# Kernel optimization log

Hardware: AMD Instinct MI355X
Metric: run time of the kernel (lower is better)

Reference implementation:

```python
import jax, jax.numpy as jnp
import numpy as np

N, D, H, C, K = 16384, 128, 128, 10, 32  # cells, in-dim, hidden, classes, kNN neighbors


def setup_inputs() -> dict:
    key = jax.random.key(0)
    k0, k1, k2 = jax.random.split(key, 3)
    return {
        "X": jax.random.normal(k0, (N, D), dtype=jnp.float32),
        "W1": jax.random.normal(k1, (2 * D, H), dtype=jnp.float32) * 0.05,
        "b1": jnp.zeros((H,), dtype=jnp.float32),
        "W2": jax.random.normal(k2, (2 * H, C), dtype=jnp.float32) * 0.05,
        "b2": jnp.zeros((C,), dtype=jnp.float32),
    }


def _knn_idx(X, k):
    # knn_graph(X, k, loop=True): k nearest neighbors incl. self per node
    sq = jnp.sum(X * X, axis=1)
    d2 = sq[:, None] - 2.0 * (X @ X.T) + sq[None, :]  # [N, N] squared dists
    _, idx = jax.lax.top_k(-d2, k)  # [N, k] neighbor indices (self has d2=0)
    return idx


def _edge_conv(X, idx, W, b, relu):
    # PyG EdgeConv: out_i = max_j mlp(concat(x_i, x_j - x_i))
    xi = X[:, None, :]                 # [N, 1, d]
    xj = X[idx]                        # [N, k, d] gather
    msg = jnp.concatenate([jnp.broadcast_to(xi, xj.shape), xj - xi], axis=-1)
    h = msg @ W + b                    # [N, k, out]
    if relu:
        h = jax.nn.relu(h)
    return jnp.max(h, axis=1)          # max aggregation over neighbors


def reference(X, W1, b1, W2, b2):
    # dropout p=0.0 -> identity
    idx = _knn_idx(X, K)               # graph built once, reused (edge_index cached)
    h = _edge_conv(X, idx, W1, b1, relu=True)
    out = _edge_conv(h, idx, W2, b2, relu=False)
    return out
```

## Files before the change

### kernel.cpp

```cpp
#include <hip/hip_runtime.h>
#include <math.h>

#define Nn 16384
#define Dd 128
#define Kk 32
#define JSPLIT 8
#define JCH (Nn / JSPLIT)
#define NG (JCH / 16)
#define CAP 32
#define MAXSLOT 2
#define BAND 0.4f
#define ZQ 2.4176f

typedef unsigned short u16;
typedef short short8 __attribute__((ext_vector_type(8)));
typedef float f32x4 __attribute__((ext_vector_type(4)));

__device__ __forceinline__ u16 f2bf(float x) {
    unsigned u = __float_as_uint(x);
    unsigned r = u + 0x7FFFu + ((u >> 16) & 1u);
    return (u16)(r >> 16);
}

__global__ __launch_bounds__(256) void prep_kernel(const float* __restrict__ X,
                                                   u16* __restrict__ Xhi,
                                                   float* __restrict__ sqn,
                                                   float* __restrict__ thrA,
                                                   int* __restrict__ flagCnt) {
    const int i = blockIdx.x * 4 + (threadIdx.x >> 6);
    const int lane = threadIdx.x & 63;
    const float2 v = *(const float2*)(X + (size_t)i * Dd + lane * 2);
    const unsigned pack = ((unsigned)f2bf(v.y) << 16) | (unsigned)f2bf(v.x);
    *(unsigned*)(Xhi + (size_t)i * Dd + lane * 2) = pack;
    float s = fmaf(v.x, v.x, v.y * v.y);
#pragma unroll
    for (int o = 32; o > 0; o >>= 1) s += __shfl_down(s, o);
    if (lane == 0) {
        sqn[i] = s;
        thrA[i] = 128.0f - ZQ * sqrtf(256.0f + 4.0f * s);
    }
    if (blockIdx.x == 0 && threadIdx.x == 0) *flagCnt = 0;
}

__global__ __launch_bounds__(256, 2) void knn_filter(const u16* __restrict__ Xhi,
                                                     const float* __restrict__ sqn,
                                                     const float* __restrict__ thrA,
                                                     u16* __restrict__ cand,
                                                     int* __restrict__ candCnt) {
    __shared__ u16 listF[256 * CAP + 256];
    __shared__ int cntS[256];

    const int tid = threadIdx.x;
    const int wave = tid >> 6, lane = tid & 63;
    const int quad = lane >> 4, n16 = lane & 15;
    const int itile = blockIdx.x >> 3, chunk = blockIdx.x & 7;
    const int ibase = itile * 256;
    const int wbase = ibase + wave * 64;
    const int jch0 = chunk * JCH;
    const unsigned below = (1u << n16) - 1u;
    const int scrapOff = 256 * CAP + tid;

    short8 aF[4][4];
#pragma unroll
    for (int is = 0; is < 4; is++) {
        const u16* arow = Xhi + (size_t)(wbase + is * 16 + n16) * Dd + quad * 8;
#pragma unroll
        for (int ks = 0; ks < 4; ks++) aF[is][ks] = *(const short8*)(arow + ks * 32);
    }
    float nhT[16];
    int cntReg[16];
#pragma unroll
    for (int is = 0; is < 4; is++)
#pragma unroll
        for (int r = 0; r < 4; r++) {
            nhT[is * 4 + r] = -0.5f * thrA[wbase + is * 16 + quad * 4 + r];
            cntReg[is * 4 + r] = 0;
        }

    const u16* bbase = Xhi + (size_t)(jch0 + n16) * Dd + quad * 8;
    short8 bb[2][4];
    float sj[2];
#pragma unroll
    for (int ks = 0; ks < 4; ks++) bb[0][ks] = *(const short8*)(bbase + ks * 32);
    sj[0] = sqn[jch0 + n16];
#pragma unroll
    for (int ks = 0; ks < 4; ks++) bb[1][ks] = *(const short8*)(bbase + 16 * Dd + ks * 32);
    sj[1] = sqn[jch0 + 16 + n16];

#define MSTEP(p, gg)                                                           \
    {                                                                          \
        const float bias = -0.5f * sj[p];                                      \
        acc##p[0] = (f32x4){bias, bias, bias, bias};                           \
        acc##p[1] = acc##p[0]; acc##p[2] = acc##p[0]; acc##p[3] = acc##p[0];   \
        _Pragma("unroll")                                                      \
        for (int ks = 0; ks < 4; ks++) {                                       \
            acc##p[0] = __builtin_amdgcn_mfma_f32_16x16x32_bf16(aF[0][ks], bb[p][ks], acc##p[0], 0, 0, 0); \
            acc##p[1] = __builtin_amdgcn_mfma_f32_16x16x32_bf16(aF[1][ks], bb[p][ks], acc##p[1], 0, 0, 0); \
            acc##p[2] = __builtin_amdgcn_mfma_f32_16x16x32_bf16(aF[2][ks], bb[p][ks], acc##p[2], 0, 0, 0); \
            acc##p[3] = __builtin_amdgcn_mfma_f32_16x16x32_bf16(aF[3][ks], bb[p][ks], acc##p[3], 0, 0, 0); \
        }                                                                      \
        {      \
            const u16* nb = bbase + (size_t)((gg) + 2) * 16 * Dd;              \
            bb[p][0] = *(const short8*)(nb);                                   \
            bb[p][1] = *(const short8*)(nb + 32);                              \
            bb[p][2] = *(const short8*)(nb + 64);                              \
            bb[p][3] = *(const short8*)(nb + 96);                              \
            sj[p] = sqn[jch0 + ((gg) + 2) * 16 + n16];                         \
        }                                                                      \
    }

#define TSTEP(p, gg)                                                           \
    {                                                                          \
        const int jj = jch0 + (gg) * 16 + n16;                                 \
        _Pragma("unroll")                                                      \
        for (int is = 0; is < 4; is++) {                                       \
            _Pragma("unroll")                                                  \
            for (int r = 0; r < 4; r++) {                                      \
                const int ir = is * 4 + r;                                     \
                const bool h = acc##p[is][r] > nhT[ir];                        \
                const unsigned long long mr = __ballot(h);                     \
                const unsigned qm = (unsigned)(mr >> (quad * 16)) & 0xFFFFu;   \
                const int pos = cntReg[ir] + __popc(qm & below);               \
                const bool wr = h && (pos < CAP);                              \
                const int rowbase = (wave * 64 + is * 16 + quad * 4 + r) * CAP; \
                const int off = wr ? rowbase + pos : scrapOff;                 \
                listF[off] = (u16)jj;        \
                cntReg[ir] += __popc(qm);                                      \
            }                                                                  \
        }                                                                      \
    }

    f32x4 acc0[4], acc1[4];
    MSTEP(0, 0)
    for (int g = 0; g < NG - 2; g += 2) {
        MSTEP(1, g + 1)
        TSTEP(0, g)
        MSTEP(0, g + 2)
        TSTEP(1, g + 1)
    }
    MSTEP(1, NG - 1)
    TSTEP(0, NG - 2)
    TSTEP(1, NG - 1)
#undef MSTEP
#undef TSTEP

    if (n16 == 0) {
#pragma unroll
        for (int is = 0; is < 4; is++)
#pragma unroll
            for (int r = 0; r < 4; r++)
                cntS[wave * 64 + is * 16 + quad * 4 + r] = cntReg[is * 4 + r];
    }
    for (int rl = 0; rl < 64; rl++) {
        const int row = wave * 64 + rl;
        const int n = cntS[row];
        const int gi = ibase + row;
        if (lane == 0) candCnt[(size_t)gi * JSPLIT + chunk] = n;
        if (lane < min(n, CAP))
            cand[((size_t)gi * JSPLIT + chunk) * CAP + lane] = listF[row * CAP + lane];
    }
}

__global__ __launch_bounds__(256) void knn_exact(const float* __restrict__ X,
                                                 const float* __restrict__ sqn,
                                                 const float* __restrict__ thrA,
                                                 const u16* __restrict__ cand,
                                                 const int* __restrict__ candCnt,
                                                 int* __restrict__ idx_out,
                                                 int* __restrict__ flagCnt,
                                                 int* __restrict__ flagRows) {
    const int wave = threadIdx.x >> 6, lane = threadIdx.x & 63;
    const int quad = lane >> 4, n16 = lane & 15;
    const int i = blockIdx.x * 4 + wave;

    float4 xi[8];
    {
        const float4* xb = (const float4*)(X + (size_t)i * Dd + quad * 32);
#pragma unroll
        for (int u = 0; u < 8; u++) xi[u] = xb[u];
    }
    int pre[JSPLIT];
    bool over = false;
    int M = 0;
#pragma unroll
    for (int k = 0; k < JSPLIT; k++) {
        int c = candCnt[(size_t)i * JSPLIT + k];
        over = over || (c > CAP);
        pre[k] = M;
        M += min(c, CAP);
    }
    over = over || (M > 64 * MAXSLOT);
    if (over) {
        if (lane == 0) { const int f = atomicAdd(flagCnt, 1); flagRows[f] = i; }
        return;
    }
    const float rvT = thrA[i];

    float rv[MAXSLOT];
    int jd[MAXSLOT];
#pragma unroll
    for (int s = 0; s < MAXSLOT; s++) { rv[s] = INFINITY; jd[s] = -1; }

#pragma unroll
    for (int s = 0; s < MAXSLOT; s++) {
#pragma unroll
        for (int t = 0; t < 4; t++) {
            const int c = s * 64 + t * 16 + n16;
            if (c < M) {
                int k = 0;
#pragma unroll
                for (int q = 1; q < JSPLIT; q++) if (c >= pre[q]) k = q;
                const int jj = cand[((size_t)i * JSPLIT + k) * CAP + (c - pre[k])];
                const float4* xb = (const float4*)(X + (size_t)jj * Dd + quad * 32);
                float s0 = 0.f, s1 = 0.f, s2 = 0.f, s3 = 0.f;
#pragma unroll
                for (int u = 0; u < 8; u++) {
                    const float4 b = xb[u];
                    s0 = fmaf(xi[u].x, b.x, s0); s1 = fmaf(xi[u].y, b.y, s1);
                    s2 = fmaf(xi[u].z, b.z, s2); s3 = fmaf(xi[u].w, b.w, s3);
                }
                float p = (s0 + s1) + (s2 + s3);
                p += __shfl_xor(p, 16);
                p += __shfl_xor(p, 32);
                if (quad == t) { rv[s] = fmaf(-2.f, p, sqn[jj]); jd[s] = jj; }
            }
        }
    }

    int good = 0;
#pragma unroll
    for (int s = 0; s < MAXSLOT; s++) good += __popcll(__ballot(rv[s] < rvT - BAND));
    if (good < Kk) {
        if (lane == 0) { const int f = atomicAdd(flagCnt, 1); flagRows[f] = i; }
        return;
    }
    int rk[MAXSLOT] = {};
    for (int s2 = 0; s2 < 64; s2++) {
        float ov[MAXSLOT];
#pragma unroll
        for (int s = 0; s < MAXSLOT; s++) ov[s] = __shfl(rv[s], s2);
#pragma unroll
        for (int s = 0; s < MAXSLOT; s++) {
            const int myid = lane + 64 * s;
#pragma unroll
            for (int t = 0; t < MAXSLOT; t++)
                rk[s] += (ov[t] < rv[s] || (ov[t] == rv[s] && s2 + 64 * t < myid)) ? 1 : 0;
        }
    }
#pragma unroll
    for (int s = 0; s < MAXSLOT; s++)
        if (jd[s] >= 0 && rk[s] < Kk) idx_out[(size_t)i * Kk + rk[s]] = jd[s];
}

__global__ __launch_bounds__(256) void knn_cleanup(const float* __restrict__ X,
                                                   const float* __restrict__ sqn,
                                                   const int* __restrict__ flagCnt,
                                                   const int* __restrict__ flagRows,
                                                   float* __restrict__ scratch,
                                                   int* __restrict__ idx_out) {
    __shared__ float xi[Dd];
    __shared__ int cntS;
    __shared__ float lv[256];
    __shared__ int lj[256];
    const int tid = threadIdx.x;
    const int lane = tid & 63;
    const int F = *flagCnt;
    float* rvS = scratch + (size_t)blockIdx.x * Nn;
    for (int f = blockIdx.x; f < F; f += gridDim.x) {
        const int i = flagRows[f];
        __syncthreads();
        if (tid < Dd) xi[tid] = X[(size_t)i * Dd + tid];
        __syncthreads();
        for (int j = tid; j < Nn; j += 256) {
            const float* xj = X + (size_t)j * Dd;
            float s0 = 0.f, s1 = 0.f, s2 = 0.f, s3 = 0.f;
#pragma unroll
            for (int d = 0; d < Dd; d += 4) {
                const float4 a = *(const float4*)&xi[d];
                const float4 b = *(const float4*)(xj + d);
                s0 = fmaf(a.x, b.x, s0); s1 = fmaf(a.y, b.y, s1);
                s2 = fmaf(a.z, b.z, s2); s3 = fmaf(a.w, b.w, s3);
            }
            rvS[j] = fmaf(-2.f, (s0 + s1) + (s2 + s3), sqn[j]);
        }
        __syncthreads();
        float lo = -1.0e9f, hi = 1.0e9f, T = 1.0e9f;
        for (int it = 0; it < 48; it++) {
            const float mid = 0.5f * (lo + hi);
            int local = 0;
            for (int j = tid; j < Nn; j += 256) local += (rvS[j] < mid) ? 1 : 0;
#pragma unroll
            for (int o = 32; o > 0; o >>= 1) local += __shfl_down(local, o);
            __syncthreads();
            if (tid == 0) cntS = 0;
            __syncthreads();
            if (lane == 0) atomicAdd(&cntS, local);
            __syncthreads();
            const int c = cntS;
            if (c < Kk) lo = mid;
            else if (c > 200) hi = mid;
            else { T = mid; break; }
        }
        if (T == 1.0e9f) T = hi;
        __syncthreads();
        if (tid == 0) cntS = 0;
        __syncthreads();
        for (int j = tid; j < Nn; j += 256) {
            if (rvS[j] < T) {
                const int p = atomicAdd(&cntS, 1);
                if (p < 256) { lv[p] = rvS[j]; lj[p] = j; }
            }
        }
        __syncthreads();
        const int n = min(cntS, 256);
        if (tid < 64) {
            float v[4]; int jjj[4]; int rk2[4] = {0, 0, 0, 0};
#pragma unroll
            for (int s = 0; s < 4; s++) {
                const int sl = lane + 64 * s;
                v[s] = (sl < n) ? lv[sl] : INFINITY;
                jjj[s] = (sl < n) ? lj[sl] : -1;
            }
            for (int s2 = 0; s2 < 64; s2++) {
                const float o0 = __shfl(v[0], s2), o1 = __shfl(v[1], s2);
                const float o2 = __shfl(v[2], s2), o3 = __shfl(v[3], s2);
#pragma unroll
                for (int s = 0; s < 4; s++) {
                    const int myid = lane + 64 * s;
                    rk2[s] += (o0 < v[s] || (o0 == v[s] && s2 < myid));
                    rk2[s] += (o1 < v[s] || (o1 == v[s] && s2 + 64 < myid));
                    rk2[s] += (o2 < v[s] || (o2 == v[s] && s2 + 128 < myid));
                    rk2[s] += (o3 < v[s] || (o3 == v[s] && s2 + 192 < myid));
                }
            }
#pragma unroll
            for (int s = 0; s < 4; s++)
                if (jjj[s] >= 0 && rk2[s] < Kk) idx_out[(size_t)i * Kk + rk2[s]] = jjj[s];
        }
        __syncthreads();
    }
}

__global__ __launch_bounds__(256) void pq_kernel(const float* __restrict__ X,
                                                 const float* __restrict__ W1,
                                                 const float* __restrict__ b1,
                                                 float* __restrict__ P,
                                                 float* __restrict__ Q) {
    __shared__ float xrow[16][Dd];
    const int i0 = blockIdx.x * 16;
    for (int t = threadIdx.x; t < 16 * Dd / 4; t += 256)
        ((float4*)&xrow[0][0])[t] = ((const float4*)(X + (size_t)i0 * Dd))[t];
    __syncthreads();
    const int cc = threadIdx.x & 127;
    const int mat = threadIdx.x >> 7;
    float acc[16];
#pragma unroll
    for (int r = 0; r < 16; r++) acc[r] = 0.f;
    for (int d = 0; d < Dd; d++) {
        float w;
        if (mat == 0) w = W1[d * 128 + cc] - W1[(128 + d) * 128 + cc];
        else          w = W1[(128 + d) * 128 + cc];
#pragma unroll
        for (int r = 0; r < 16; r++) acc[r] = fmaf(xrow[r][d], w, acc[r]);
    }
    if (mat == 0) {
        const float b = b1[cc];
#pragma unroll
        for (int r = 0; r < 16; r++) P[(size_t)(i0 + r) * 128 + cc] = acc[r] + b;
    } else {
#pragma unroll
        for (int r = 0; r < 16; r++) Q[(size_t)(i0 + r) * 128 + cc] = acc[r];
    }
}

__global__ __launch_bounds__(128) void h1_kernel(const float* __restrict__ P,
                                                 const float* __restrict__ Q,
                                                 const int* __restrict__ idx,
                                                 float* __restrict__ h1) {
    const int i = blockIdx.x;
    const int c = threadIdx.x;
    __shared__ int jb[Kk];
    if (threadIdx.x < Kk) jb[threadIdx.x] = idx[(size_t)i * Kk + threadIdx.x];
    __syncthreads();
    float m = -INFINITY;
#pragma unroll
    for (int k = 0; k < Kk; k++) m = fmaxf(m, Q[(size_t)jb[k] * 128 + c]);
    h1[(size_t)i * 128 + c] = fmaxf(P[(size_t)i * 128 + c] + m, 0.f);
}

__global__ __launch_bounds__(256) void pq2_kernel(const float* __restrict__ h1,
                                                  const float* __restrict__ W2,
                                                  const float* __restrict__ b2,
                                                  float* __restrict__ P2,
                                                  float* __restrict__ Q2) {
    __shared__ float w2s[2560];
    __shared__ float h1s[16][132];
    const int i0 = blockIdx.x * 16;
    for (int t = threadIdx.x; t < 640; t += 256)
        ((float4*)w2s)[t] = ((const float4*)W2)[t];
    {
        const int r = threadIdx.x >> 4, q = (threadIdx.x & 15) * 8;
        *(float4*)&h1s[r][q]     = *(const float4*)(h1 + (size_t)(i0 + r) * 128 + q);
        *(float4*)&h1s[r][q + 4] = *(const float4*)(h1 + (size_t)(i0 + r) * 128 + q + 4);
    }
    __syncthreads();
    const int il = threadIdx.x >> 4, c = threadIdx.x & 15;
    if (c >= 10) return;
    float pa = 0.f, pb = 0.f;
#pragma unroll 4
    for (int d = 0; d < Dd; d++) {
        const float h = h1s[il][d];
        const float wa = w2s[d * 10 + c];
        const float wb = w2s[(128 + d) * 10 + c];
        pa = fmaf(h, wa - wb, pa);
        pb = fmaf(h, wb, pb);
    }
    P2[(size_t)(i0 + il) * 10 + c] = pa + b2[c];
    Q2[(size_t)(i0 + il) * 10 + c] = pb;
}

__global__ __launch_bounds__(256) void out_kernel(const float* __restrict__ P2,
                                                  const float* __restrict__ Q2,
                                                  const int* __restrict__ idx,
                                                  float* __restrict__ out) {
    const int g = blockIdx.x * 256 + threadIdx.x;
    const int i = g >> 4;
    const int c = g & 15;
    if (c >= 10) return;
    const int* jr = idx + (size_t)i * Kk;
    float m = -INFINITY;
#pragma unroll
    for (int k = 0; k < Kk; k++) m = fmaxf(m, Q2[(size_t)jr[k] * 10 + c]);
    out[(size_t)i * 10 + c] = P2[(size_t)i * 10 + c] + m;
}

extern "C" void kernel_launch(void* const* d_in, const int* in_sizes, int n_in,
                              void* d_out, int out_size, void* d_ws, size_t ws_size,
                              hipStream_t stream) {
    const float* X  = (const float*)d_in[0];
    const float* W1 = (const float*)d_in[1];
    const float* b1 = (const float*)d_in[2];
    const float* W2 = (const float*)d_in[3];
    const float* b2 = (const float*)d_in[4];
    float* out = (float*)d_out;

    char* ws = (char*)d_ws;
    float* sqn     = (float*)(ws + 0);
    float* thrA    = (float*)(ws + 73728);
    int*   flagCnt = (int*)(ws + 139264);
    int*   flagRows= (int*)(ws + 139392);
    int*   idx     = (int*)(ws + 262144);
    u16*   Xhi     = (u16*)(ws + 2359296);
    float* P       = (float*)(ws + 6561792);
    float* Q       = P + (size_t)Nn * 128;
    float* h1      = Q + (size_t)Nn * 128;
    float* P2      = h1 + (size_t)Nn * 128;
    float* Q2      = P2 + (size_t)Nn * 10;
    u16* cand    = (u16*)P;
    int* candCnt = (int*)((char*)P + 13631488);
    float* cleanupScratch = P;

    prep_kernel<<<Nn / 4, 256, 0, stream>>>(X, Xhi, sqn, thrA, flagCnt);
    knn_filter<<<64 * JSPLIT, 256, 0, stream>>>(Xhi, sqn, thrA, cand, candCnt);
    knn_exact<<<Nn / 4, 256, 0, stream>>>(X, sqn, thrA, cand, candCnt, idx, flagCnt, flagRows);
    knn_cleanup<<<256, 256, 0, stream>>>(X, sqn, flagCnt, flagRows, cleanupScratch, idx);
    pq_kernel<<<Nn / 16, 256, 0, stream>>>(X, W1, b1, P, Q);
    h1_kernel<<<Nn, 128, 0, stream>>>(P, Q, idx, h1);
    pq2_kernel<<<Nn / 16, 256, 0, stream>>>(h1, W2, b2, P2, Q2);
    out_kernel<<<Nn * 16 / 256, 256, 0, stream>>>(P2, Q2, idx, out);
}
```

Baseline: 382.6 us.

## Prune exact kNN candidates using stored approximate scores; fuse h1 into pq2

The filter kernel now also stores each candidate's bf16 MFMA dot product as fp16. The exact kernel ranks candidates by that approximate score, finds the 32nd-best value, and computes exact fp32 distances only for candidates within a fixed margin of it, cutting gathers of neighbour rows. Separately, h1_kernel is folded into pq2_kernel so the neighbour max, ReLU and second projection run in one pass without writing h1 to memory, and pq_kernel handles 32 rows per block. The fixed margin is heuristic: it can drop true neighbours when the approximation error exceeds it, and the 64-step shuffle ranking adds per-row work.

```diff
diff --git a/kernel.cpp b/kernel.cpp
--- a/kernel.cpp
+++ b/kernel.cpp
@@ -10,6 +10,7 @@
 #define CAP 32
 #define MAXSLOT 2
 #define BAND 0.4f
+#define PMARG 1.0f
 #define ZQ 2.4176f
 
 typedef unsigned short u16;
@@ -46,8 +47,10 @@
                                                      const float* __restrict__ sqn,
                                                      const float* __restrict__ thrA,
                                                      u16* __restrict__ cand,
+                                                     u16* __restrict__ apxG,
                                                      int* __restrict__ candCnt) {
     __shared__ u16 listF[256 * CAP + 256];
+    __shared__ u16 accS[256 * CAP + 256];
     __shared__ int cntS[256];
 
     const int tid = threadIdx.x;
@@ -117,7 +120,8 @@
             _Pragma("unroll")                                                  \
             for (int r = 0; r < 4; r++) {                                      \
                 const int ir = is * 4 + r;                                     \
-                const bool h = acc##p[is][r] > nhT[ir];                        \
+                const float av = acc##p[is][r];                                \
+                const bool h = av > nhT[ir];                                   \
                 const unsigned long long mr = __ballot(h);                     \
                 const unsigned qm = (unsigned)(mr >> (quad * 16)) & 0xFFFFu;   \
                 const int pos = cntReg[ir] + __popc(qm & below);               \
@@ -125,6 +129,7 @@
                 const int rowbase = (wave * 64 + is * 16 + quad * 4 + r) * CAP; \
                 const int off = wr ? rowbase + pos : scrapOff;                 \
                 listF[off] = (u16)jj;        \
+                accS[off] = __builtin_bit_cast(unsigned short, (_Float16)av);  \
                 cntReg[ir] += __popc(qm);                                      \
             }                                                                  \
         }                                                                      \
@@ -156,8 +161,11 @@
         const int n = cntS[row];
         const int gi = ibase + row;
         if (lane == 0) candCnt[(size_t)gi * JSPLIT + chunk] = n;
-        if (lane < min(n, CAP))
-            cand[((size_t)gi * JSPLIT + chunk) * CAP + lane] = listF[row * CAP + lane];
+        if (lane < min(n, CAP)) {
+            const size_t o = ((size_t)gi * JSPLIT + chunk) * CAP + lane;
+            cand[o] = listF[row * CAP + lane];
+            apxG[o] = accS[row * CAP + lane];
+        }
     }
 }
 
@@ -165,10 +173,12 @@
                                                  const float* __restrict__ sqn,
                                                  const float* __restrict__ thrA,
                                                  const u16* __restrict__ cand,
+                                                 const u16* __restrict__ apxG,
                                                  const int* __restrict__ candCnt,
                                                  int* __restrict__ idx_out,
                                                  int* __restrict__ flagCnt,
                                                  int* __restrict__ flagRows) {
+    __shared__ u16 sjd[4][128];
     const int wave = threadIdx.x >> 6, lane = threadIdx.x & 63;
     const int quad = lane >> 4, n16 = lane & 15;
     const int i = blockIdx.x * 4 + wave;
@@ -196,6 +206,56 @@
     }
     const float rvT = thrA[i];
 
+    float ra[MAXSLOT];
+    int jdA[MAXSLOT];
+#pragma unroll
+    for (int s = 0; s < MAXSLOT; s++) {
+        const int c = s * 64 + lane;
+        if (c < M) {
+            int k = 0;
+#pragma unroll
+            for (int q = 1; q < JSPLIT; q++) if (c >= pre[q]) k = q;
+            const size_t o = ((size_t)i * JSPLIT + k) * CAP + (c - pre[k]);
+            jdA[s] = cand[o];
+            const _Float16 hf = __builtin_bit_cast(_Float16, apxG[o]);
+            ra[s] = -2.0f * (float)hf;
+        } else { ra[s] = INFINITY; jdA[s] = -1; }
+    }
+    int rkA[MAXSLOT] = {};
+    for (int s2 = 0; s2 < 64; s2++) {
+        const float o0 = __shfl(ra[0], s2), o1 = __shfl(ra[1], s2);
+#pragma unroll
+        for (int s = 0; s < MAXSLOT; s++) {
+            const int myid = lane + 64 * s;
+            rkA[s] += (o0 < ra[s] || (o0 == ra[s] && s2 < myid)) ? 1 : 0;
+            rkA[s] += (o1 < ra[s] || (o1 == ra[s] && s2 + 64 < myid)) ? 1 : 0;
+        }
+    }
+    float t32 = INFINITY;
+    if (M >= Kk) {
+        const unsigned long long m0 = __ballot(rkA[0] == Kk - 1);
+        if (m0) t32 = __shfl(ra[0], __ffsll(m0) - 1);
+        else {
+            const unsigned long long m1 = __ballot(rkA[1] == Kk - 1);
+            t32 = __shfl(ra[1], __ffsll(m1) - 1);
+        }
+    }
+    const float wEnd = t32 + PMARG;
+
+    int ns;
+    {
+        const bool sel0 = ra[0] <= wEnd;
+        const unsigned long long b0 = __ballot(sel0);
+        const int c0 = __popcll(b0);
+        const int p0 = __popcll(b0 & ((1ull << lane) - 1ull));
+        const bool sel1 = ra[1] <= wEnd;
+        const unsigned long long b1 = __ballot(sel1);
+        const int p1 = c0 + __popcll(b1 & ((1ull << lane) - 1ull));
+        ns = c0 + __popcll(b1);
+        if (sel0) sjd[wave][p0] = (u16)jdA[0];
+        if (sel1) sjd[wave][p1] = (u16)jdA[1];
+    }
+
     float rv[MAXSLOT];
     int jd[MAXSLOT];
 #pragma unroll
@@ -206,11 +266,8 @@
 #pragma unroll
         for (int t = 0; t < 4; t++) {
             const int c = s * 64 + t * 16 + n16;
-            if (c < M) {
-                int k = 0;
-#pragma unroll
-                for (int q = 1; q < JSPLIT; q++) if (c >= pre[q]) k = q;
-                const int jj = cand[((size_t)i * JSPLIT + k) * CAP + (c - pre[k])];
+            if (c < ns) {
+                const int jj = sjd[wave][c];
                 const float4* xb = (const float4*)(X + (size_t)jj * Dd + quad * 32);
                 float s0 = 0.f, s1 = 0.f, s2 = 0.f, s3 = 0.f;
 #pragma unroll
@@ -346,65 +403,74 @@
                                                  const float* __restrict__ b1,
                                                  float* __restrict__ P,
                                                  float* __restrict__ Q) {
-    __shared__ float xrow[16][Dd];
-    const int i0 = blockIdx.x * 16;
-    for (int t = threadIdx.x; t < 16 * Dd / 4; t += 256)
+    __shared__ float xrow[32][Dd];
+    const int i0 = blockIdx.x * 32;
+    for (int t = threadIdx.x; t < 32 * Dd / 4; t += 256)
         ((float4*)&xrow[0][0])[t] = ((const float4*)(X + (size_t)i0 * Dd))[t];
     __syncthreads();
     const int cc = threadIdx.x & 127;
     const int mat = threadIdx.x >> 7;
-    float acc[16];
-#pragma unroll
-    for (int r = 0; r < 16; r++) acc[r] = 0.f;
+    float acc[32];
+#pragma unroll
+    for (int r = 0; r < 32; r++) acc[r] = 0.f;
     for (int d = 0; d < Dd; d++) {
         float w;
         if (mat == 0) w = W1[d * 128 + cc] - W1[(128 + d) * 128 + cc];
         else          w = W1[(128 + d) * 128 + cc];
 #pragma unroll
-        for (int r = 0; r < 16; r++) acc[r] = fmaf(xrow[r][d], w, acc[r]);
+        for (int r = 0; r < 32; r++) acc[r] = fmaf(xrow[r][d], w, acc[r]);
     }
     if (mat == 0) {
         const float b = b1[cc];
 #pragma unroll
-        for (int r = 0; r < 16; r++) P[(size_t)(i0 + r) * 128 + cc] = acc[r] + b;
+        for (int r = 0; r < 32; r++) P[(size_t)(i0 + r) * 128 + cc] = acc[r] + b;
     } else {
 #pragma unroll
-        for (int r = 0; r < 16; r++) Q[(size_t)(i0 + r) * 128 + cc] = acc[r];
-    }
-}
-
-__global__ __launch_bounds__(128) void h1_kernel(const float* __restrict__ P,
-                                                 const float* __restrict__ Q,
-                                                 const int* __restrict__ idx,
-                                                 float* __restrict__ h1) {
-    const int i = blockIdx.x;
-    const int c = threadIdx.x;
-    __shared__ int jb[Kk];
-    if (threadIdx.x < Kk) jb[threadIdx.x] = idx[(size_t)i * Kk + threadIdx.x];
-    __syncthreads();
-    float m = -INFINITY;
-#pragma unroll
-    for (int k = 0; k < Kk; k++) m = fmaxf(m, Q[(size_t)jb[k] * 128 + c]);
-    h1[(size_t)i * 128 + c] = fmaxf(P[(size_t)i * 128 + c] + m, 0.f);
-}
-
-__global__ __launch_bounds__(256) void pq2_kernel(const float* __restrict__ h1,
+        for (int r = 0; r < 32; r++) Q[(size_t)(i0 + r) * 128 + cc] = acc[r];
+    }
+}
+
+__global__ __launch_bounds__(256) void pq2_kernel(const float* __restrict__ P,
+                                                  const float* __restrict__ Q,
+                                                  const int* __restrict__ idx,
                                                   const float* __restrict__ W2,
                                                   const float* __restrict__ b2,
                                                   float* __restrict__ P2,
                                                   float* __restrict__ Q2) {
     __shared__ float w2s[2560];
     __shared__ float h1s[16][132];
+    __shared__ int jbS[16][Kk];
     const int i0 = blockIdx.x * 16;
-    for (int t = threadIdx.x; t < 640; t += 256)
+    const int tid = threadIdx.x;
+    for (int t = tid; t < 640; t += 256)
         ((float4*)w2s)[t] = ((const float4*)W2)[t];
+    ((int2*)&jbS[0][0])[tid] = ((const int2*)(idx + (size_t)i0 * Kk))[tid];
+    __syncthreads();
     {
-        const int r = threadIdx.x >> 4, q = (threadIdx.x & 15) * 8;
-        *(float4*)&h1s[r][q]     = *(const float4*)(h1 + (size_t)(i0 + r) * 128 + q);
-        *(float4*)&h1s[r][q + 4] = *(const float4*)(h1 + (size_t)(i0 + r) * 128 + q + 4);
+        const int r = tid >> 4, c0 = (tid & 15) * 8;
+        float4 m0 = {-INFINITY, -INFINITY, -INFINITY, -INFINITY}, m1 = m0;
+        for (int k = 0; k < Kk; k++) {
+            const int jb = jbS[r][k];
+            const float4* qb = (const float4*)(Q + (size_t)jb * 128 + c0);
+            const float4 a = qb[0], b = qb[1];
+            m0.x = fmaxf(m0.x, a.x); m0.y = fmaxf(m0.y, a.y);
+            m0.z = fmaxf(m0.z, a.z); m0.w = fmaxf(m0.w, a.w);
+            m1.x = fmaxf(m1.x, b.x); m1.y = fmaxf(m1.y, b.y);
+            m1.z = fmaxf(m1.z, b.z); m1.w = fmaxf(m1.w, b.w);
+        }
+        const float4* pb = (const float4*)(P + (size_t)(i0 + r) * 128 + c0);
+        const float4 pa = pb[0], pc = pb[1];
+        h1s[r][c0 + 0] = fmaxf(pa.x + m0.x, 0.f);
+        h1s[r][c0 + 1] = fmaxf(pa.y + m0.y, 0.f);
+        h1s[r][c0 + 2] = fmaxf(pa.z + m0.z, 0.f);
+        h1s[r][c0 + 3] = fmaxf(pa.w + m0.w, 0.f);
+        h1s[r][c0 + 4] = fmaxf(pc.x + m1.x, 0.f);
+        h1s[r][c0 + 5] = fmaxf(pc.y + m1.y, 0.f);
+        h1s[r][c0 + 6] = fmaxf(pc.z + m1.z, 0.f);
+        h1s[r][c0 + 7] = fmaxf(pc.w + m1.w, 0.f);
     }
     __syncthreads();
-    const int il = threadIdx.x >> 4, c = threadIdx.x & 15;
+    const int il = tid >> 4, c = tid & 15;
     if (c >= 10) return;
     float pa = 0.f, pb = 0.f;
 #pragma unroll 4
@@ -453,19 +519,18 @@
     u16*   Xhi     = (u16*)(ws + 2359296);
     float* P       = (float*)(ws + 6561792);
     float* Q       = P + (size_t)Nn * 128;
-    float* h1      = Q + (size_t)Nn * 128;
-    float* P2      = h1 + (size_t)Nn * 128;
+    float* P2      = P + (size_t)3 * Nn * 128;
     float* Q2      = P2 + (size_t)Nn * 10;
     u16* cand    = (u16*)P;
-    int* candCnt = (int*)((char*)P + 13631488);
+    u16* apxG    = (u16*)Q;
+    int* candCnt = (int*)((char*)P + (size_t)2 * Nn * 128 * 4);
     float* cleanupScratch = P;
 
     prep_kernel<<<Nn / 4, 256, 0, stream>>>(X, Xhi, sqn, thrA, flagCnt);
-    knn_filter<<<64 * JSPLIT, 256, 0, stream>>>(Xhi, sqn, thrA, cand, candCnt);
-    knn_exact<<<Nn / 4, 256, 0, stream>>>(X, sqn, thrA, cand, candCnt, idx, flagCnt, flagRows);
+    knn_filter<<<64 * JSPLIT, 256, 0, stream>>>(Xhi, sqn, thrA, cand, apxG, candCnt);
+    knn_exact<<<Nn / 4, 256, 0, stream>>>(X, sqn, thrA, cand, apxG, candCnt, idx, flagCnt, flagRows);
     knn_cleanup<<<256, 256, 0, stream>>>(X, sqn, flagCnt, flagRows, cleanupScratch, idx);
-    pq_kernel<<<Nn / 16, 256, 0, stream>>>(X, W1, b1, P, Q);
-    h1_kernel<<<Nn, 128, 0, stream>>>(P, Q, idx, h1);
-    pq2_kernel<<<Nn / 16, 256, 0, stream>>>(h1, W2, b2, P2, Q2);
+    pq_kernel<<<Nn / 32, 256, 0, stream>>>(X, W1, b1, P, Q);
+    pq2_kernel<<<Nn / 16, 256, 0, stream>>>(P, Q, idx, W2, b2, P2, Q2);
     out_kernel<<<Nn * 16 / 256, 256, 0, stream>>>(P2, Q2, idx, out);
 }
```

After: 377.0 us. About the same (-1.5%).
